# Optimization experiments

Measured on AMD Instinct MI355X. Metric: run time of the kernel, lower is better.

Reference implementation:

```python
import jax, jax.numpy as jnp
import numpy as np

B, T, C, H = 4, 4096, 1024, 16

def setup_inputs() -> dict:
    key = jax.random.key(0)
    k1, k2, k3, k4 = jax.random.split(key, 4)
    return {
        "x": jax.random.normal(k1, (B, T, C), dtype=jnp.float32),
        "W_attn": jax.random.normal(k2, (C, C), dtype=jnp.float32) * 0.02,
        "b_attn": jnp.zeros((C,), dtype=jnp.float32),
        "W_proj": jax.random.normal(k3, (C, C), dtype=jnp.float32) * 0.02,
        "b_proj": jnp.zeros((C,), dtype=jnp.float32),
        "temp": jnp.ones((H, 1), dtype=jnp.float32),
        "n_head": H,
    }

def reference(x, W_attn, b_attn, W_proj, b_proj, temp, n_head):
    Bb, Tt, Cc = x.shape
    D = Cc // n_head
    # c_attn (torch Linear: x @ W.T + b)
    w = x @ W_attn.T + b_attn                         # (B,T,C)
    w = w.reshape(Bb, Tt, n_head, D).transpose(0, 2, 1, 3)  # (B,H,T,D)
    # F.normalize over token axis (dim=-2), eps=1e-12
    norm = jnp.maximum(jnp.sqrt(jnp.sum(w * w, axis=-2, keepdims=True)), 1e-12)
    w_normed = w / norm
    tmp = jnp.sum(w_normed ** 2, axis=-1) * temp      # (B,H,T) * (H,1) -> (B,H,T)
    Pi = jax.nn.softmax(tmp, axis=1)                  # softmax over heads
    Pi_prob = Pi / (jnp.sum(Pi, axis=-1, keepdims=True) + 1e-8)  # (B,H,T)
    dots = jnp.einsum('bht,bhtd->bhd', Pi_prob, w ** 2)          # (B,H,D)
    attn = 1.0 / (1.0 + dots)                         # (B,H,D)
    y = -(w * Pi[..., None]) * attn[:, :, None, :]    # (B,H,T,D)
    y = y.transpose(0, 2, 1, 3).reshape(Bb, Tt, Cc)
    return y @ W_proj.T + b_proj
```

## Files before the change

### kernel.cpp

```cpp
#include <hip/hip_runtime.h>
#include <hip/hip_bf16.h>

#define BB 4
#define TT 4096
#define CC 1024
#define HH 16
#define DD 64

typedef __attribute__((ext_vector_type(8))) short short8;
typedef __attribute__((ext_vector_type(8))) __bf16 bf16x8;
typedef __attribute__((ext_vector_type(4))) float f32x4;

static __device__ __forceinline__ unsigned short f2bf(float f) {
    unsigned int u = __builtin_bit_cast(unsigned int, f);
    unsigned int r = (u + 0x7FFFu + ((u >> 16) & 1u)) >> 16;
    return (unsigned short)r;
}
static __device__ __forceinline__ float bf2f(unsigned short h) {
    return __builtin_bit_cast(float, ((unsigned int)h) << 16);
}
static __device__ __forceinline__ bf16x8 cvt8(f32x4 a, f32x4 b) {
    bf16x8 r;
    r[0] = (__bf16)a[0]; r[1] = (__bf16)a[1]; r[2] = (__bf16)a[2]; r[3] = (__bf16)a[3];
    r[4] = (__bf16)b[0]; r[5] = (__bf16)b[1]; r[6] = (__bf16)b[2]; r[7] = (__bf16)b[3];
    return r;
}

__global__ void k_f32_to_bf16(const float* __restrict__ src,
                              unsigned short* __restrict__ dst, int n4) {
    int i = blockIdx.x * 256 + threadIdx.x;
    if (i >= n4) return;
    float4 v = ((const float4*)src)[i];
    ushort4 o;
    o.x = f2bf(v.x); o.y = f2bf(v.y); o.z = f2bf(v.z); o.w = f2bf(v.w);
    ((ushort4*)dst)[i] = o;
}

static __device__ __forceinline__ void stage_b16_512(
    const unsigned short* __restrict__ Gbase, unsigned short* lbase,
    int k0, int K, int wave, int lane)
{
    #pragma unroll
    for (int q = 0; q < 2; ++q) {
        int c = (wave * 2 + q) * 64 + lane;
        int r = c >> 2;
        int j = c & 3;
        int srcj = (j - (r >> 1)) & 3;
        const unsigned short* g = Gbase + (size_t)r * K + k0 + srcj * 8;
        __builtin_amdgcn_global_load_lds(
            (const __attribute__((address_space(1))) void*)g,
            (__attribute__((address_space(3))) void*)(lbase + (wave * 2 + q) * 512),
            16, 0, 0);
    }
}

static __device__ __forceinline__ void stage_a32_512(
    const float* __restrict__ Gbase, unsigned short* lbase,
    int k0, int K, int wave, int lane)
{
    #pragma unroll
    for (int q = 0; q < 4; ++q) {
        int c = q * 512 + wave * 64 + lane;
        int r = c >> 3;
        int j = c & 7;
        int srcj = (j - r) & 7;
        const float* g = Gbase + (size_t)r * K + k0 + srcj * 4;
        __builtin_amdgcn_global_load_lds(
            (const __attribute__((address_space(1))) void*)g,
            (__attribute__((address_space(3))) void*)(lbase + (q * 512 + wave * 64) * 8),
            16, 0, 0);
    }
}

__global__ __launch_bounds__(512, 2)
void k_gemm1(const float* __restrict__ X,
             const unsigned short* __restrict__ B,
             const float* __restrict__ bias,
             unsigned short* __restrict__ Cout,
             float* __restrict__ S,
             int M, int N, int K)
{
    __shared__ unsigned short lds[3][24576];
    const int tid  = threadIdx.x;
    const int wave = tid >> 6;
    const int lane = tid & 63;
    const int wr = wave >> 2, wc = wave & 3;
    const int fr = lane & 15, hi = lane >> 4;

    const int wg  = blockIdx.x;
    const int swz = (wg & 7) * 32 + (wg >> 3);
    const int bn  = swz & 3;
    const int bm  = swz >> 2;
    const int b   = bm >> 4;

    const float* Af32 = X + (size_t)(bm * 256) * K;
    const unsigned short* Bbase = B + (size_t)(bn * 256) * K;
    const int nt = K / 32;

    const int slB  = (hi + (fr >> 1)) & 3;
    const int boff = 16384 + (wc * 64 + fr) * 32 + slB * 8;
    const int sl0   = (2 * hi + fr) & 7;
    const int sl1   = (2 * hi + 1 + fr) & 7;
    const int arowf = (wr * 128 + fr) * 32;

    f32x4 acc[8][4] = {};

    stage_a32_512(Af32, lds[0],          0,  K, wave, lane);
    stage_b16_512(Bbase, lds[0] + 16384, 0,  K, wave, lane);
    stage_a32_512(Af32, lds[1],          32, K, wave, lane);
    stage_b16_512(Bbase, lds[1] + 16384, 32, K, wave, lane);

    int rb = 0;
    for (int kt = 0; kt < nt; ++kt) {
        const unsigned short* buf = lds[rb];
        unsigned short* sbuf = lds[(rb == 0) ? 2 : rb - 1];
        int ks = kt + 2; if (ks >= nt) ks = nt - 1;
        asm volatile("s_waitcnt vmcnt(6)" ::: "memory");
        __builtin_amdgcn_s_barrier();

        bf16x8 af[8]; short8 bfr[4];
        #pragma unroll
        for (int i = 0; i < 4; ++i) bfr[i] = *(const short8*)&buf[boff + i * 512];
        const float* fbuf = (const float*)buf;
        #pragma unroll
        for (int mi = 0; mi < 8; ++mi)
            af[mi] = cvt8(*(const f32x4*)&fbuf[arowf + mi * 512 + sl0 * 4],
                          *(const f32x4*)&fbuf[arowf + mi * 512 + sl1 * 4]);

        stage_a32_512(Af32, sbuf,          ks * 32, K, wave, lane);
        stage_b16_512(Bbase, sbuf + 16384, ks * 32, K, wave, lane);

        __builtin_amdgcn_s_setprio(1);
        #pragma unroll
        for (int mi = 0; mi < 8; ++mi)
            #pragma unroll
            for (int ni = 0; ni < 4; ++ni)
                acc[mi][ni] = __builtin_amdgcn_mfma_f32_16x16x32_bf16(
                    af[mi], __builtin_bit_cast(bf16x8, bfr[ni]),
                    acc[mi][ni], 0, 0, 0);
        __builtin_amdgcn_s_setprio(0);

        rb = (rb == 2) ? 0 : rb + 1;
    }

    __syncthreads();

    const int cg = fr;
    const int rg = hi * 4;
    float* sblk = (float*)&lds[0][0];
    if (tid < 256) sblk[tid] = 0.f;
    __syncthreads();
    float csum[4] = {};
    #pragma unroll
    for (int mi = 0; mi < 8; ++mi) {
        #pragma unroll
        for (int ni = 0; ni < 4; ++ni) {
            int col = bn * 256 + wc * 64 + ni * 16 + cg;
            float bv = bias[col];
            #pragma unroll
            for (int j = 0; j < 4; ++j) {
                int row = bm * 256 + wr * 128 + mi * 16 + rg + j;
                float v = acc[mi][ni][j] + bv;
                Cout[(size_t)row * N + col] = f2bf(v);
                csum[ni] += v * v;
            }
        }
    }
    #pragma unroll
    for (int ni = 0; ni < 4; ++ni)
        atomicAdd(&sblk[wc * 64 + ni * 16 + cg], csum[ni]);
    __syncthreads();
    if (tid < 256) atomicAdd(&S[b * CC + bn * 256 + tid], sblk[tid]);
}

static __device__ __forceinline__ void stage_b16_256(
    const unsigned short* __restrict__ Gbase, unsigned short* lbase,
    int k0, int K, int tid)
{
    #pragma unroll
    for (int q = 0; q < 2; ++q) {
        int c = q * 256 + tid;
        int r = c >> 2;
        int j = c & 3;
        int srcj = (j - (r >> 1)) & 3;
        const unsigned short* g = Gbase + (size_t)r * K + k0 + srcj * 8;
        __builtin_amdgcn_global_load_lds(
            (const __attribute__((address_space(1))) void*)g,
            (__attribute__((address_space(3))) void*)(lbase + c * 8), 16, 0, 0);
    }
}

__global__ __launch_bounds__(256, 2)
void k_gemm2(const unsigned short* __restrict__ A,
             const unsigned short* __restrict__ B,
             const float* __restrict__ bias,
             float* __restrict__ Cout,
             int M, int N, int K)
{
    __shared__ unsigned short lds[8192];
    const int tid  = threadIdx.x;
    const int wave = tid >> 6;
    const int lane = tid & 63;
    const int wr = wave >> 1, wc = wave & 1;
    const int fr = lane & 15, hi = lane >> 4;

    const int wg  = blockIdx.x;
    const int swz = (wg & 7) * 128 + (wg >> 3);
    const int bn  = swz & 7;
    const int bm  = swz >> 3;
    const int b   = bm >> 5;

    const unsigned short* Abase = A + (size_t)(bm * 128) * K;
    const unsigned short* Bbase = B + ((size_t)(b * N + bn * 128)) * K;
    const int nt = K / 32;

    const int slB  = (hi + (fr >> 1)) & 3;
    const int aoff = (wr * 64 + fr) * 32 + slB * 8;
    const int boff = 4096 + (wc * 64 + fr) * 32 + slB * 8;

    f32x4 acc[4][4] = {};

    for (int kt = 0; kt < nt; ++kt) {
        const int k0 = kt * 32;
        stage_b16_256(Abase, lds,        k0, K, tid);
        stage_b16_256(Bbase, lds + 4096, k0, K, tid);
        __syncthreads();

        bf16x8 af[4]; short8 bfr[4];
        #pragma unroll
        for (int i = 0; i < 4; ++i) bfr[i] = *(const short8*)&lds[boff + i * 512];
        #pragma unroll
        for (int mi = 0; mi < 4; ++mi)
            af[mi] = __builtin_bit_cast(bf16x8, *(const short8*)&lds[aoff + mi * 512]);

        #pragma unroll
        for (int mi = 0; mi < 4; ++mi)
            #pragma unroll
            for (int ni = 0; ni < 4; ++ni)
                acc[mi][ni] = __builtin_amdgcn_mfma_f32_16x16x32_bf16(
                    af[mi], __builtin_bit_cast(bf16x8, bfr[ni]),
                    acc[mi][ni], 0, 0, 0);
        __syncthreads();
    }

    const int cg = fr;
    const int rg = hi * 4;
    #pragma unroll
    for (int mi = 0; mi < 4; ++mi) {
        #pragma unroll
        for (int ni = 0; ni < 4; ++ni) {
            int col = bn * 128 + wc * 64 + ni * 16 + cg;
            float bv = bias[col];
            #pragma unroll
            for (int j = 0; j < 4; ++j) {
                int row = bm * 128 + wr * 64 + mi * 16 + rg + j;
                Cout[(size_t)row * N + col] = acc[mi][ni][j] + bv;
            }
        }
    }
}

__global__ __launch_bounds__(256)
void k_row_softmax(unsigned short* __restrict__ w16, const float* __restrict__ S,
                   const float* __restrict__ temp,
                   float* __restrict__ dotsU, float* __restrict__ sumPi)
{
    __shared__ float dots_local[CC];
    __shared__ float sPi_local[HH];
    const int tid  = threadIdx.x;
    const int wave = tid >> 6;
    const int lane = tid & 63;
    const int bb   = blockIdx.x >> 7;
    const int tile = blockIdx.x & 127;

    for (int c = tid; c < CC; c += 256) dots_local[c] = 0.f;
    if (tid < HH) sPi_local[tid] = 0.f;
    __syncthreads();

    const int g3 = lane >> 3;
    const int li = lane & 7;

    float inv[2][8], tsc[2];
    #pragma unroll
    for (int q = 0; q < 2; ++q) {
        int c = q * 512 + lane * 8;
        const float4* sp = (const float4*)&S[bb * CC + c];
        float4 s0 = sp[0], s1 = sp[1];
        inv[q][0] = 1.f / fmaxf(s0.x, 1e-24f); inv[q][1] = 1.f / fmaxf(s0.y, 1e-24f);
        inv[q][2] = 1.f / fmaxf(s0.z, 1e-24f); inv[q][3] = 1.f / fmaxf(s0.w, 1e-24f);
        inv[q][4] = 1.f / fmaxf(s1.x, 1e-24f); inv[q][5] = 1.f / fmaxf(s1.y, 1e-24f);
        inv[q][6] = 1.f / fmaxf(s1.z, 1e-24f); inv[q][7] = 1.f / fmaxf(s1.w, 1e-24f);
        tsc[q] = temp[q * 8 + g3];
    }

    float dacc[2][8] = {};
    float sPiAcc[2] = {};

    for (int i = 0; i < 8; ++i) {
        int t = tile * 32 + wave * 8 + i;
        unsigned short* row = w16 + ((size_t)bb * TT + t) * CC;
        float wf[2][8];
        float pq[2];
        #pragma unroll
        for (int q = 0; q < 2; ++q) {
            short8 v = *(const short8*)&row[q * 512 + lane * 8];
            float s = 0.f;
            #pragma unroll
            for (int j = 0; j < 8; ++j) {
                wf[q][j] = bf2f((unsigned short)v[j]);
                s += wf[q][j] * wf[q][j] * inv[q][j];
            }
            pq[q] = s;
        }
        #pragma unroll
        for (int off = 1; off < 8; off <<= 1) {
            pq[0] += __shfl_xor(pq[0], off);
            pq[1] += __shfl_xor(pq[1], off);
        }
        pq[0] *= tsc[0]; pq[1] *= tsc[1];
        float mx = fmaxf(pq[0], pq[1]);
        mx = fmaxf(mx, __shfl_xor(mx, 8));
        mx = fmaxf(mx, __shfl_xor(mx, 16));
        mx = fmaxf(mx, __shfl_xor(mx, 32));
        float e0 = __expf(pq[0] - mx), e1 = __expf(pq[1] - mx);
        float ss = e0 + e1;
        ss += __shfl_xor(ss, 8);
        ss += __shfl_xor(ss, 16);
        ss += __shfl_xor(ss, 32);
        float rs = 1.f / ss;
        float piv[2] = { e0 * rs, e1 * rs };
        #pragma unroll
        for (int q = 0; q < 2; ++q) {
            short8 yo;
            #pragma unroll
            for (int j = 0; j < 8; ++j) {
                dacc[q][j] += piv[q] * wf[q][j] * wf[q][j];
                yo[j] = (short)f2bf(-wf[q][j] * piv[q]);
            }
            *(short8*)&row[q * 512 + lane * 8] = yo;
            if (li == 0) sPiAcc[q] += piv[q];
        }
    }

    #pragma unroll
    for (int q = 0; q < 2; ++q) {
        int c = q * 512 + lane * 8;
        #pragma unroll
        for (int j = 0; j < 8; ++j)
            atomicAdd(&dots_local[c + j], dacc[q][j]);
        if (li == 0) atomicAdd(&sPi_local[q * 8 + g3], sPiAcc[q]);
    }
    __syncthreads();
    for (int c = tid; c < CC; c += 256) atomicAdd(&dotsU[bb * CC + c], dots_local[c]);
    if (tid < HH) atomicAdd(&sumPi[bb * HH + tid], sPi_local[tid]);
}

__global__ void k_scale_wproj(const float* __restrict__ Wp,
                              const float* __restrict__ dotsU,
                              const float* __restrict__ sumPi,
                              unsigned short* __restrict__ out)
{
    int i = blockIdx.x * 256 + threadIdx.x;
    int bq  = i >> 18;
    int rem = i & 262143;
    int n   = rem >> 8;
    int cg  = (rem & 255) * 4;
    float4 wv = *(const float4*)&Wp[n * CC + cg];
    float4 du = *(const float4*)&dotsU[bq * CC + cg];
    float sp = sumPi[bq * HH + (cg >> 6)] + 1e-8f;
    float a0 = 1.f / (1.f + du.x / sp);
    float a1 = 1.f / (1.f + du.y / sp);
    float a2 = 1.f / (1.f + du.z / sp);
    float a3 = 1.f / (1.f + du.w / sp);
    ushort4 o;
    o.x = f2bf(wv.x * a0); o.y = f2bf(wv.y * a1);
    o.z = f2bf(wv.z * a2); o.w = f2bf(wv.w * a3);
    *(ushort4*)&out[((size_t)bq * CC + n) * CC + cg] = o;
}

extern "C" void kernel_launch(void* const* d_in, const int* in_sizes, int n_in,
                              void* d_out, int out_size, void* d_ws, size_t ws_size,
                              hipStream_t stream) {
    const float* x      = (const float*)d_in[0];
    const float* W_attn = (const float*)d_in[1];
    const float* b_attn = (const float*)d_in[2];
    const float* W_proj = (const float*)d_in[3];
    const float* b_proj = (const float*)d_in[4];
    const float* temp   = (const float*)d_in[5];

    char* ws = (char*)d_ws;
    unsigned short* w16   = (unsigned short*)(ws);
    unsigned short* Wa16  = (unsigned short*)(ws + 33554432);
    unsigned short* Wp16b = (unsigned short*)(ws + 35651584);
    float* S     = (float*)(ws + 44040192);
    float* dotsU = (float*)(ws + 44056576);
    float* sumPi = (float*)(ws + 44072960);

    k_f32_to_bf16<<<dim3(1024), dim3(256), 0, stream>>>(W_attn, Wa16, 262144);

    hipMemsetAsync(S, 0, 16384 + 16384 + 256, stream);

    k_gemm1<<<dim3(256), dim3(512), 0, stream>>>(
        x, Wa16, b_attn, w16, S, BB * TT, CC, CC);

    k_row_softmax<<<dim3(512), dim3(256), 0, stream>>>(w16, S, temp, dotsU, sumPi);

    k_scale_wproj<<<dim3(4096), dim3(256), 0, stream>>>(W_proj, dotsU, sumPi, Wp16b);

    k_gemm2<<<dim3(1024), dim3(256), 0, stream>>>(
        w16, Wp16b, b_proj, (float*)d_out, BB * TT, CC, CC);
}
```

Before: 128.8 us.

## Convert A to bf16 in registers, retile gemm2 to 256x256 pipelined, fuse memset

GEMM1 now loads fp32 activations into registers, converts them to bf16 and writes them to LDS. It replaces the fp32 direct-to-LDS staging and the per-MFMA conversion, which halves LDS footprint per stage and allows 4-stage buffering. GEMM2 moves from a 128x128 single-buffered tile to a 256x256 tile with 512 threads and a 4-stage global_load_lds pipeline, for better reuse and overlap. The memset is folded into the weight-conversion kernel to save a launch. The risks are register pressure from the staging registers and fewer workgroups in GEMM2 (256).

```diff
diff --git a/kernel.cpp b/kernel.cpp
--- a/kernel.cpp
+++ b/kernel.cpp
@@ -19,24 +19,27 @@
 static __device__ __forceinline__ float bf2f(unsigned short h) {
     return __builtin_bit_cast(float, ((unsigned int)h) << 16);
 }
-static __device__ __forceinline__ bf16x8 cvt8(f32x4 a, f32x4 b) {
-    bf16x8 r;
-    r[0] = (__bf16)a[0]; r[1] = (__bf16)a[1]; r[2] = (__bf16)a[2]; r[3] = (__bf16)a[3];
-    r[4] = (__bf16)b[0]; r[5] = (__bf16)b[1]; r[6] = (__bf16)b[2]; r[7] = (__bf16)b[3];
-    return r;
-}
-
-__global__ void k_f32_to_bf16(const float* __restrict__ src,
-                              unsigned short* __restrict__ dst, int n4) {
+static __device__ __forceinline__ short8 pack8(f32x4 a, f32x4 b) {
+    bf16x8 t;
+    t[0] = (__bf16)a[0]; t[1] = (__bf16)a[1]; t[2] = (__bf16)a[2]; t[3] = (__bf16)a[3];
+    t[4] = (__bf16)b[0]; t[5] = (__bf16)b[1]; t[6] = (__bf16)b[2]; t[7] = (__bf16)b[3];
+    return __builtin_bit_cast(short8, t);
+}
+
+__global__ void k_conv_and_zero(const float* __restrict__ src,
+                                unsigned short* __restrict__ dst,
+                                float* __restrict__ zbuf ) {
     int i = blockIdx.x * 256 + threadIdx.x;
-    if (i >= n4) return;
-    float4 v = ((const float4*)src)[i];
-    ushort4 o;
-    o.x = f2bf(v.x); o.y = f2bf(v.y); o.z = f2bf(v.z); o.w = f2bf(v.w);
-    ((ushort4*)dst)[i] = o;
-}
-
-static __device__ __forceinline__ void stage_b16_512(
+    if (i < 262144) {
+        float4 v = ((const float4*)src)[i];
+        ushort4 o;
+        o.x = f2bf(v.x); o.y = f2bf(v.y); o.z = f2bf(v.z); o.w = f2bf(v.w);
+        ((ushort4*)dst)[i] = o;
+    }
+    if (i < 8256) zbuf[i] = 0.f;
+}
+
+static __device__ __forceinline__ void stage_b16(
     const unsigned short* __restrict__ Gbase, unsigned short* lbase,
     int k0, int K, int wave, int lane)
 {
@@ -54,33 +57,15 @@
     }
 }
 
-static __device__ __forceinline__ void stage_a32_512(
-    const float* __restrict__ Gbase, unsigned short* lbase,
-    int k0, int K, int wave, int lane)
-{
-    #pragma unroll
-    for (int q = 0; q < 4; ++q) {
-        int c = q * 512 + wave * 64 + lane;
-        int r = c >> 3;
-        int j = c & 7;
-        int srcj = (j - r) & 7;
-        const float* g = Gbase + (size_t)r * K + k0 + srcj * 4;
-        __builtin_amdgcn_global_load_lds(
-            (const __attribute__((address_space(1))) void*)g,
-            (__attribute__((address_space(3))) void*)(lbase + (q * 512 + wave * 64) * 8),
-            16, 0, 0);
-    }
-}
-
 __global__ __launch_bounds__(512, 2)
 void k_gemm1(const float* __restrict__ X,
-             const unsigned short* __restrict__ B,
+             const unsigned short* __restrict__ Bw,
              const float* __restrict__ bias,
              unsigned short* __restrict__ Cout,
              float* __restrict__ S,
              int M, int N, int K)
 {
-    __shared__ unsigned short lds[3][24576];
+    __shared__ unsigned short lds[4][16384];
     const int tid  = threadIdx.x;
     const int wave = tid >> 6;
     const int lane = tid & 63;
@@ -94,41 +79,61 @@
     const int b   = bm >> 4;
 
     const float* Af32 = X + (size_t)(bm * 256) * K;
-    const unsigned short* Bbase = B + (size_t)(bn * 256) * K;
+    const unsigned short* Bbase = Bw + (size_t)(bn * 256) * K;
     const int nt = K / 32;
 
+    const int c0 = wave * 128 + lane;
+    const int c1 = c0 + 64;
+    const int r0 = c0 >> 2, sj0 = ((c0 & 3) - (r0 >> 1)) & 3;
+    const int r1 = c1 >> 2, sj1 = ((c1 & 3) - (r1 >> 1)) & 3;
+    const float* aG0 = Af32 + (size_t)r0 * K + sj0 * 8;
+    const float* aG1 = Af32 + (size_t)r1 * K + sj1 * 8;
+
     const int slB  = (hi + (fr >> 1)) & 3;
-    const int boff = 16384 + (wc * 64 + fr) * 32 + slB * 8;
-    const int sl0   = (2 * hi + fr) & 7;
-    const int sl1   = (2 * hi + 1 + fr) & 7;
-    const int arowf = (wr * 128 + fr) * 32;
+    const int aoff = (wr * 128 + fr) * 32 + slB * 8;
+    const int boff = 8192 + (wc * 64 + fr) * 32 + slB * 8;
 
     f32x4 acc[8][4] = {};
-
-    stage_a32_512(Af32, lds[0],          0,  K, wave, lane);
-    stage_b16_512(Bbase, lds[0] + 16384, 0,  K, wave, lane);
-    stage_a32_512(Af32, lds[1],          32, K, wave, lane);
-    stage_b16_512(Bbase, lds[1] + 16384, 32, K, wave, lane);
-
-    int rb = 0;
+    f32x4 rA0, rA1, rA2, rA3;
+
+    {
+        f32x4 t00, t01, t02, t03, t10, t11, t12, t13, t20, t21, t22, t23;
+        t00 = *(const f32x4*)(aG0 +  0); t01 = *(const f32x4*)(aG0 +  4);
+        t02 = *(const f32x4*)(aG1 +  0); t03 = *(const f32x4*)(aG1 +  4);
+        t10 = *(const f32x4*)(aG0 + 32); t11 = *(const f32x4*)(aG0 + 36);
+        t12 = *(const f32x4*)(aG1 + 32); t13 = *(const f32x4*)(aG1 + 36);
+        t20 = *(const f32x4*)(aG0 + 64); t21 = *(const f32x4*)(aG0 + 68);
+        t22 = *(const f32x4*)(aG1 + 64); t23 = *(const f32x4*)(aG1 + 68);
+        stage_b16(Bbase, lds[0] + 8192,  0, K, wave, lane);
+        stage_b16(Bbase, lds[1] + 8192, 32, K, wave, lane);
+        stage_b16(Bbase, lds[2] + 8192, 64, K, wave, lane);
+        *(short8*)&lds[0][c0 * 8] = pack8(t00, t01);
+        *(short8*)&lds[0][c1 * 8] = pack8(t02, t03);
+        *(short8*)&lds[1][c0 * 8] = pack8(t10, t11);
+        *(short8*)&lds[1][c1 * 8] = pack8(t12, t13);
+        *(short8*)&lds[2][c0 * 8] = pack8(t20, t21);
+        *(short8*)&lds[2][c1 * 8] = pack8(t22, t23);
+    }
+    asm volatile("s_waitcnt lgkmcnt(0)" ::: "memory");
+
     for (int kt = 0; kt < nt; ++kt) {
-        const unsigned short* buf = lds[rb];
-        unsigned short* sbuf = lds[(rb == 0) ? 2 : rb - 1];
-        int ks = kt + 2; if (ks >= nt) ks = nt - 1;
-        asm volatile("s_waitcnt vmcnt(6)" ::: "memory");
+        const unsigned short* buf = lds[kt & 3];
+        unsigned short* sbuf = lds[(kt + 3) & 3];
+        int ks = kt + 3; if (ks >= nt) ks = nt - 1;
+
+        asm volatile("s_waitcnt vmcnt(4)" ::: "memory");
         __builtin_amdgcn_s_barrier();
 
-        bf16x8 af[8]; short8 bfr[4];
+        short8 af[8], bfr[4];
         #pragma unroll
         for (int i = 0; i < 4; ++i) bfr[i] = *(const short8*)&buf[boff + i * 512];
-        const float* fbuf = (const float*)buf;
-        #pragma unroll
-        for (int mi = 0; mi < 8; ++mi)
-            af[mi] = cvt8(*(const f32x4*)&fbuf[arowf + mi * 512 + sl0 * 4],
-                          *(const f32x4*)&fbuf[arowf + mi * 512 + sl1 * 4]);
-
-        stage_a32_512(Af32, sbuf,          ks * 32, K, wave, lane);
-        stage_b16_512(Bbase, sbuf + 16384, ks * 32, K, wave, lane);
+        #pragma unroll
+        for (int mi = 0; mi < 8; ++mi) af[mi] = *(const short8*)&buf[aoff + mi * 512];
+
+        const int kf = ks * 32;
+        rA0 = *(const f32x4*)(aG0 + kf); rA1 = *(const f32x4*)(aG0 + kf + 4);
+        rA2 = *(const f32x4*)(aG1 + kf); rA3 = *(const f32x4*)(aG1 + kf + 4);
+        stage_b16(Bbase, sbuf + 8192, kf, K, wave, lane);
 
         __builtin_amdgcn_s_setprio(1);
         #pragma unroll
@@ -136,11 +141,14 @@
             #pragma unroll
             for (int ni = 0; ni < 4; ++ni)
                 acc[mi][ni] = __builtin_amdgcn_mfma_f32_16x16x32_bf16(
-                    af[mi], __builtin_bit_cast(bf16x8, bfr[ni]),
+                    __builtin_bit_cast(bf16x8, af[mi]),
+                    __builtin_bit_cast(bf16x8, bfr[ni]),
                     acc[mi][ni], 0, 0, 0);
         __builtin_amdgcn_s_setprio(0);
 
-        rb = (rb == 2) ? 0 : rb + 1;
+        *(short8*)&sbuf[c0 * 8] = pack8(rA0, rA1);
+        *(short8*)&sbuf[c1 * 8] = pack8(rA2, rA3);
+        asm volatile("s_waitcnt lgkmcnt(0)" ::: "memory");
     }
 
     __syncthreads();
@@ -173,87 +181,85 @@
     if (tid < 256) atomicAdd(&S[b * CC + bn * 256 + tid], sblk[tid]);
 }
 
-static __device__ __forceinline__ void stage_b16_256(
-    const unsigned short* __restrict__ Gbase, unsigned short* lbase,
-    int k0, int K, int tid)
-{
-    #pragma unroll
-    for (int q = 0; q < 2; ++q) {
-        int c = q * 256 + tid;
-        int r = c >> 2;
-        int j = c & 3;
-        int srcj = (j - (r >> 1)) & 3;
-        const unsigned short* g = Gbase + (size_t)r * K + k0 + srcj * 8;
-        __builtin_amdgcn_global_load_lds(
-            (const __attribute__((address_space(1))) void*)g,
-            (__attribute__((address_space(3))) void*)(lbase + c * 8), 16, 0, 0);
-    }
-}
-
-__global__ __launch_bounds__(256, 2)
+__global__ __launch_bounds__(512, 2)
 void k_gemm2(const unsigned short* __restrict__ A,
              const unsigned short* __restrict__ B,
              const float* __restrict__ bias,
              float* __restrict__ Cout,
              int M, int N, int K)
 {
-    __shared__ unsigned short lds[8192];
+    __shared__ unsigned short lds[4][16384];
     const int tid  = threadIdx.x;
     const int wave = tid >> 6;
     const int lane = tid & 63;
-    const int wr = wave >> 1, wc = wave & 1;
+    const int wr = wave >> 2, wc = wave & 3;
     const int fr = lane & 15, hi = lane >> 4;
 
     const int wg  = blockIdx.x;
-    const int swz = (wg & 7) * 128 + (wg >> 3);
-    const int bn  = swz & 7;
-    const int bm  = swz >> 3;
-    const int b   = bm >> 5;
-
-    const unsigned short* Abase = A + (size_t)(bm * 128) * K;
-    const unsigned short* Bbase = B + ((size_t)(b * N + bn * 128)) * K;
+    const int swz = (wg & 7) * 32 + (wg >> 3);
+    const int bn  = swz & 3;
+    const int bm  = swz >> 2;
+    const int b   = bm >> 4;
+
+    const unsigned short* Abase = A + (size_t)(bm * 256) * K;
+    const unsigned short* Bbase = B + ((size_t)(b * N + bn * 256)) * K;
     const int nt = K / 32;
 
     const int slB  = (hi + (fr >> 1)) & 3;
-    const int aoff = (wr * 64 + fr) * 32 + slB * 8;
-    const int boff = 4096 + (wc * 64 + fr) * 32 + slB * 8;
-
-    f32x4 acc[4][4] = {};
+    const int aoff = (wr * 128 + fr) * 32 + slB * 8;
+    const int boff = 8192 + (wc * 64 + fr) * 32 + slB * 8;
+
+    f32x4 acc[8][4] = {};
+
+    stage_b16(Abase, lds[0],        0,  K, wave, lane);
+    stage_b16(Bbase, lds[0] + 8192, 0,  K, wave, lane);
+    stage_b16(Abase, lds[1],        32, K, wave, lane);
+    stage_b16(Bbase, lds[1] + 8192, 32, K, wave, lane);
+    stage_b16(Abase, lds[2],        64, K, wave, lane);
+    stage_b16(Bbase, lds[2] + 8192, 64, K, wave, lane);
 
     for (int kt = 0; kt < nt; ++kt) {
-        const int k0 = kt * 32;
-        stage_b16_256(Abase, lds,        k0, K, tid);
-        stage_b16_256(Bbase, lds + 4096, k0, K, tid);
-        __syncthreads();
-
-        bf16x8 af[4]; short8 bfr[4];
-        #pragma unroll
-        for (int i = 0; i < 4; ++i) bfr[i] = *(const short8*)&lds[boff + i * 512];
-        #pragma unroll
-        for (int mi = 0; mi < 4; ++mi)
-            af[mi] = __builtin_bit_cast(bf16x8, *(const short8*)&lds[aoff + mi * 512]);
-
-        #pragma unroll
-        for (int mi = 0; mi < 4; ++mi)
+        const unsigned short* buf = lds[kt & 3];
+        unsigned short* sbuf = lds[(kt + 3) & 3];
+        int ks = kt + 3; if (ks >= nt) ks = nt - 1;
+
+        asm volatile("s_waitcnt vmcnt(8)" ::: "memory");
+        __builtin_amdgcn_s_barrier();
+
+        short8 af[8], bfr[4];
+        #pragma unroll
+        for (int i = 0; i < 4; ++i) bfr[i] = *(const short8*)&buf[boff + i * 512];
+        #pragma unroll
+        for (int mi = 0; mi < 8; ++mi) af[mi] = *(const short8*)&buf[aoff + mi * 512];
+
+        stage_b16(Abase, sbuf,        ks * 32, K, wave, lane);
+        stage_b16(Bbase, sbuf + 8192, ks * 32, K, wave, lane);
+
+        __builtin_amdgcn_s_setprio(1);
+        #pragma unroll
+        for (int mi = 0; mi < 8; ++mi)
             #pragma unroll
             for (int ni = 0; ni < 4; ++ni)
                 acc[mi][ni] = __builtin_amdgcn_mfma_f32_16x16x32_bf16(
-                    af[mi], __builtin_bit_cast(bf16x8, bfr[ni]),
+                    __builtin_bit_cast(bf16x8, af[mi]),
+                    __builtin_bit_cast(bf16x8, bfr[ni]),
                     acc[mi][ni], 0, 0, 0);
-        __syncthreads();
-    }
+        __builtin_amdgcn_s_setprio(0);
+    }
+
+    __syncthreads();
 
     const int cg = fr;
     const int rg = hi * 4;
     #pragma unroll
-    for (int mi = 0; mi < 4; ++mi) {
+    for (int mi = 0; mi < 8; ++mi) {
         #pragma unroll
         for (int ni = 0; ni < 4; ++ni) {
-            int col = bn * 128 + wc * 64 + ni * 16 + cg;
+            int col = bn * 256 + wc * 64 + ni * 16 + cg;
             float bv = bias[col];
             #pragma unroll
             for (int j = 0; j < 4; ++j) {
-                int row = bm * 128 + wr * 64 + mi * 16 + rg + j;
+                int row = bm * 256 + wr * 128 + mi * 16 + rg + j;
                 Cout[(size_t)row * N + col] = acc[mi][ni][j] + bv;
             }
         }
@@ -396,9 +402,7 @@
     float* dotsU = (float*)(ws + 44056576);
     float* sumPi = (float*)(ws + 44072960);
 
-    k_f32_to_bf16<<<dim3(1024), dim3(256), 0, stream>>>(W_attn, Wa16, 262144);
-
-    hipMemsetAsync(S, 0, 16384 + 16384 + 256, stream);
+    k_conv_and_zero<<<dim3(1024), dim3(256), 0, stream>>>(W_attn, Wa16, S);
 
     k_gemm1<<<dim3(256), dim3(512), 0, stream>>>(
         x, Wa16, b_attn, w16, S, BB * TT, CC, CC);
@@ -407,6 +411,6 @@
 
     k_scale_wproj<<<dim3(4096), dim3(256), 0, stream>>>(W_proj, dotsU, sumPi, Wp16b);
 
-    k_gemm2<<<dim3(1024), dim3(256), 0, stream>>>(
+    k_gemm2<<<dim3(256), dim3(512), 0, stream>>>(
         w16, Wp16b, b_proj, (float*)d_out, BB * TT, CC, CC);
 }
```

Measured after the change: 122.9 us. 1.05x faster.
